# Kernel optimization log

Measured on AMD Instinct MI355X. Metric: run time of the kernel, lower is better.

## Reference

```python
import jax, jax.numpy as jnp
import numpy as np

H = 2048      # hidden_size
NH = 16       # n_heads
DH = H // NH  # d_head = 128
EPS = 1e-5


def layernorm(x, w, b=None, eps=EPS):
    mu = jnp.mean(x, axis=-1, keepdims=True)
    var = jnp.mean(jnp.square(x - mu), axis=-1, keepdims=True)
    y = (x - mu) * jax.lax.rsqrt(var + eps) * w
    return y + b if b is not None else y


def rotate_half(x):
    x1, x2 = jnp.split(x, 2, axis=-1)
    return jnp.concatenate([-x2, x1], axis=-1)


def rotary_cos_sin(seq_len, dim, dtype):
    inv_freq = 1.0 / (10000.0 ** (jnp.arange(0, dim, 2, dtype=jnp.float32) / dim))
    t = jnp.arange(seq_len, dtype=jnp.float32)
    freqs = jnp.outer(t, inv_freq)            # [L, dim/2]
    emb = jnp.concatenate([freqs, freqs], -1) # [L, dim]
    return jnp.cos(emb).astype(dtype), jnp.sin(emb).astype(dtype)


def setup_inputs() -> dict:
    key = jax.random.key(0)
    ks = jax.random.split(key, 9)
    s = 0.02
    return {
        "x": jax.random.normal(ks[0], (4, 2048, H), jnp.float32),
        "ln1_w": jnp.ones((H,), jnp.float32),
        "ln1_b": jnp.zeros((H,), jnp.float32),
        "Wqkv": jax.random.normal(ks[1], (H, 3 * H), jnp.float32) * s,
        "bqkv": jnp.zeros((3 * H,), jnp.float32),
        "qln_w": jnp.ones((H,), jnp.float32),
        "kln_w": jnp.ones((H,), jnp.float32),
        "Wo": jax.random.normal(ks[2], (H, H), jnp.float32) * s,
        "bo": jnp.zeros((H,), jnp.float32),
    }


def reference(x, ln1_w, ln1_b, Wqkv, bqkv, qln_w, kln_w, Wo, bo):
    b, L, _ = x.shape
    # fused LN + QKV projection
    qkv = layernorm(x, ln1_w, ln1_b) @ Wqkv + bqkv          # [b, L, 3H]
    q, k, v = jnp.split(qkv, 3, axis=-1)
    # per-projection LayerNorm (no bias) over full hidden dim
    q = layernorm(q, qln_w).astype(qkv.dtype)
    k = layernorm(k, kln_w).astype(qkv.dtype)
    # rotary on per-head dims: [b, L, NH, DH]
    q = q.reshape(b, L, NH, DH)
    k = k.reshape(b, L, NH, DH)
    cos, sin = rotary_cos_sin(L, DH, q.dtype)
    cos = cos[None, :, None, :]
    sin = sin[None, :, None, :]
    q = q * cos + rotate_half(q) * sin
    k = k * cos + rotate_half(k) * sin
    # b s h d -> b h s d
    q = q.transpose(0, 2, 1, 3)
    k = k.transpose(0, 2, 1, 3)
    v = v.reshape(b, L, NH, DH).transpose(0, 2, 1, 3)
    # SDPA (no mask, non-causal)
    scale = 1.0 / jnp.sqrt(jnp.asarray(DH, q.dtype))
    scores = jnp.einsum('bhqd,bhkd->bhqk', q, k) * scale
    attn = jax.nn.softmax(scores, axis=-1)
    a = jnp.einsum('bhqk,bhkd->bhqd', attn, v)
    a = a.transpose(0, 2, 1, 3).reshape(b, L, H)
    return a @ Wo + bo
```

## Files before the change

kernel.cpp:

```cpp
#include <hip/hip_runtime.h>
#include <math.h>

#define HD   2048
#define NH_  16
#define DH_  128
#define SEQ_ 2048
#define B_   4
#define NT_  (B_*SEQ_)
#define EPS_ 1e-5f

typedef __attribute__((ext_vector_type(8))) __bf16 bf16x8;
typedef __attribute__((ext_vector_type(4))) __bf16 bf16x4;
typedef __attribute__((ext_vector_type(4))) float f32x4;

typedef const __attribute__((address_space(1))) void* gcptr_t;
typedef __attribute__((address_space(3))) void* lptr_t;

__device__ __forceinline__ void gload16(const void* g, void* l) {
  __builtin_amdgcn_global_load_lds((gcptr_t)g, (lptr_t)l, 16, 0, 0);
}

__device__ __forceinline__ float block_sum256(float v, float* red) {
#pragma unroll
  for (int o = 32; o > 0; o >>= 1) v += __shfl_down(v, o);
  int lane = threadIdx.x & 63, wid = threadIdx.x >> 6;
  __syncthreads();
  if (lane == 0) red[wid] = v;
  __syncthreads();
  return red[0] + red[1] + red[2] + red[3];
}

__global__ void ws_diag_kernel(float* out, float v) { out[0] = v; }

__global__ void rope_table_kernel(float* __restrict__ ct, float* __restrict__ st) {
  int i = blockIdx.x * 256 + threadIdx.x;
  if (i >= SEQ_ * 64) return;
  int l = i >> 6, d = i & 63;
  double invf = exp2(-(double)d * (13.287712379549449 / 64.0));
  double ang = (double)l * invf;
  ct[i] = (float)cos(ang);
  st[i] = (float)sin(ang);
}

template<bool LO>
__global__ __launch_bounds__(256) void ln1_split_kernel(const float* __restrict__ x,
    const float* __restrict__ w, const float* __restrict__ bias,
    __bf16* __restrict__ Ah, __bf16* __restrict__ Al) {
  __shared__ float red[4];
  int t = threadIdx.x;
  const float4* xr = (const float4*)(x + (size_t)blockIdx.x * HD);
  float4 a = xr[t], b = xr[t + 256];
  float s = a.x + a.y + a.z + a.w + b.x + b.y + b.z + b.w;
  s = block_sum256(s, red);
  float mu = s * (1.0f / HD);
  float dx[8] = {a.x - mu, a.y - mu, a.z - mu, a.w - mu,
                 b.x - mu, b.y - mu, b.z - mu, b.w - mu};
  float ss = 0.f;
#pragma unroll
  for (int i = 0; i < 8; ++i) ss += dx[i] * dx[i];
  ss = block_sum256(ss, red);
  float rs = rsqrtf(ss * (1.0f / HD) + EPS_);
  float4 w0 = ((const float4*)w)[t], w1 = ((const float4*)w)[t + 256];
  float4 b0 = ((const float4*)bias)[t], b1 = ((const float4*)bias)[t + 256];
  float y[8];
  y[0] = dx[0]*rs*w0.x + b0.x; y[1] = dx[1]*rs*w0.y + b0.y;
  y[2] = dx[2]*rs*w0.z + b0.z; y[3] = dx[3]*rs*w0.w + b0.w;
  y[4] = dx[4]*rs*w1.x + b1.x; y[5] = dx[5]*rs*w1.y + b1.y;
  y[6] = dx[6]*rs*w1.z + b1.z; y[7] = dx[7]*rs*w1.w + b1.w;
  bf16x4 h0, h1, l0, l1;
#pragma unroll
  for (int i = 0; i < 4; ++i) {
    h0[i] = (__bf16)y[i];     l0[i] = (__bf16)(y[i] - (float)h0[i]);
    h1[i] = (__bf16)y[i + 4]; l1[i] = (__bf16)(y[i + 4] - (float)h1[i]);
  }
  size_t base = (size_t)blockIdx.x * HD;
  *(bf16x4*)&Ah[base + 4 * t] = h0;
  *(bf16x4*)&Ah[base + 1024 + 4 * t] = h1;
  if (LO) {
    *(bf16x4*)&Al[base + 4 * t] = l0;
    *(bf16x4*)&Al[base + 1024 + 4 * t] = l1;
  }
}

template<bool LO>
__global__ __launch_bounds__(256) void wsplit_kernel(const float* __restrict__ W,
    int K, int N, __bf16* __restrict__ Wh, __bf16* __restrict__ Wl) {
  __shared__ float ts[64][69];
  int k0 = blockIdx.x << 6, n0 = blockIdx.y << 6;
  int t = threadIdx.x;
#pragma unroll
  for (int i = 0; i < 16; ++i) {
    int lin = t + i * 256;
    int k = lin >> 6, n = lin & 63;
    ts[k][n] = W[(size_t)(k0 + k) * N + n0 + n];
  }
  __syncthreads();
#pragma unroll
  for (int i = 0; i < 16; ++i) {
    int lin = t + i * 256;
    int n = lin >> 6, k = lin & 63;
    float v = ts[k][n];
    __bf16 h = (__bf16)v;
    size_t o = (size_t)(n0 + n) * K + k0 + k;
    Wh[o] = h;
    if (LO) Wl[o] = (__bf16)(v - (float)h);
  }
}

__global__ __launch_bounds__(256) void qkln_rope_kernel(__bf16* __restrict__ qkv,
    const float* __restrict__ qw, const float* __restrict__ kw,
    const float* __restrict__ ct, const float* __restrict__ st) {
  __shared__ float red[4];
  int t = threadIdx.x;
  int tok = blockIdx.x;
  int part = blockIdx.y;
  int pos = tok & (SEQ_ - 1);
  __bf16* base = qkv + (size_t)tok * (3 * HD) + (size_t)part * HD;
  const float* w = part ? kw : qw;
  bf16x8 v8 = *(const bf16x8*)(base + 8 * t);
  float x[8];
#pragma unroll
  for (int i = 0; i < 8; ++i) x[i] = (float)v8[i];
  float s = 0.f;
#pragma unroll
  for (int i = 0; i < 8; ++i) s += x[i];
  s = block_sum256(s, red);
  float mu = s * (1.0f / HD);
  float ss = 0.f;
#pragma unroll
  for (int i = 0; i < 8; ++i) { x[i] -= mu; ss += x[i] * x[i]; }
  ss = block_sum256(ss, red);
  float rs = rsqrtf(ss * (1.0f / HD) + EPS_);
  float4 w0 = *(const float4*)&w[8 * t];
  float4 w1 = *(const float4*)&w[8 * t + 4];
  float y[8];
  y[0] = x[0]*rs*w0.x; y[1] = x[1]*rs*w0.y; y[2] = x[2]*rs*w0.z; y[3] = x[3]*rs*w0.w;
  y[4] = x[4]*rs*w1.x; y[5] = x[5]*rs*w1.y; y[6] = x[6]*rs*w1.z; y[7] = x[7]*rs*w1.w;
  float o[8];
#pragma unroll
  for (int i = 0; i < 8; ++i) o[i] = __shfl_xor(y[i], 8);
  int d = (8 * t) & 127;
  int dd = (d < 64) ? d : d - 64;
  float4 c0 = *(const float4*)&ct[pos * 64 + dd];
  float4 c1 = *(const float4*)&ct[pos * 64 + dd + 4];
  float4 s0 = *(const float4*)&st[pos * 64 + dd];
  float4 s1 = *(const float4*)&st[pos * 64 + dd + 4];
  float cv[8] = {c0.x, c0.y, c0.z, c0.w, c1.x, c1.y, c1.z, c1.w};
  float sv[8] = {s0.x, s0.y, s0.z, s0.w, s1.x, s1.y, s1.z, s1.w};
  bf16x8 o8;
  if (d < 64) {
#pragma unroll
    for (int i = 0; i < 8; ++i) o8[i] = (__bf16)(y[i] * cv[i] - o[i] * sv[i]);
  } else {
#pragma unroll
    for (int i = 0; i < 8; ++i) o8[i] = (__bf16)(y[i] * cv[i] + o[i] * sv[i]);
  }
  *(bf16x8*)(base + 8 * t) = o8;
}

template<int TERMS, bool OUTBF16>
__global__ __launch_bounds__(256, 2) void gemm_bf3_kernel(
    const __bf16* __restrict__ Ah, const __bf16* __restrict__ Al,
    const __bf16* __restrict__ Bh, const __bf16* __restrict__ Bl,
    const float* __restrict__ bias, void* __restrict__ C,
    int M, int N, int K) {
  __shared__ __bf16 lds[TERMS + 1][128][64];
  constexpr int AL_OFF = 16384;
  constexpr int BH_OFF = (TERMS == 1) ? 16384 : 32768;
  constexpr int BL_OFF = 49152;
  const int t = threadIdx.x;
  const int lane = t & 63, wave = t >> 6;
  const int c = lane & 15, g = lane >> 4;
  const int wm = (wave & 1) << 6, wn = (wave >> 1) << 6;

  const int nwg = gridDim.x * gridDim.y;
  int lin = blockIdx.y * gridDim.x + blockIdx.x;
  int swz = (lin & 7) * (nwg >> 3) + (lin >> 3);
  const int col0 = (swz % gridDim.x) << 7;
  const int row0 = (swz / gridDim.x) << 7;

  const int srow = (wave << 5) + (lane >> 3);
  const int ch = lane & 7;
  size_t offA[4], offB[4];
#pragma unroll
  for (int i = 0; i < 4; ++i) {
    int rA = srow + i * 8;
    offA[i] = (size_t)(row0 + rA) * (K * 2) + (size_t)((ch ^ (rA & 7)) << 4);
    offB[i] = (size_t)(col0 + rA) * (K * 2) + (size_t)((ch ^ (rA & 7)) << 4);
  }
  const char* pAh = (const char*)Ah;
  const char* pAl = (const char*)Al;
  const char* pBh = (const char*)Bh;
  const char* pBl = (const char*)Bl;
  char* ldsb = (char*)&lds[0][0][0];

  float bias_[4];
#pragma unroll
  for (int nt = 0; nt < 4; ++nt) bias_[nt] = bias[col0 + wn + nt * 16 + c];

  f32x4 acc[4][4];
#pragma unroll
  for (int mt = 0; mt < 4; ++mt)
#pragma unroll
    for (int nt = 0; nt < 4; ++nt) acc[mt][nt] = f32x4{0.f, 0.f, 0.f, 0.f};

  for (int k0 = 0; k0 < K; k0 += 64) {
    const size_t k2 = (size_t)k0 * 2;
    __syncthreads();
#pragma unroll
    for (int i = 0; i < 4; ++i) {
      const int lr = (wave << 5) + (i << 3);
      gload16(pAh + offA[i] + k2, ldsb + (lr << 7));
      if (TERMS >= 2) gload16(pAl + offA[i] + k2, ldsb + AL_OFF + (lr << 7));
      gload16(pBh + offB[i] + k2, ldsb + BH_OFF + (lr << 7));
      if (TERMS == 3) gload16(pBl + offB[i] + k2, ldsb + BL_OFF + (lr << 7));
    }
    __syncthreads();
#pragma unroll
    for (int kc = 0; kc < 2; ++kc) {
      bf16x8 ah[4], al[4];
#pragma unroll
      for (int mt = 0; mt < 4; ++mt) {
        const int r = wm + mt * 16 + c;
        const int cb = (((kc << 2) | g) ^ (r & 7)) << 4;
        ah[mt] = *(const bf16x8*)(ldsb + (r << 7) + cb);
        if (TERMS >= 2) al[mt] = *(const bf16x8*)(ldsb + AL_OFF + (r << 7) + cb);
      }
#pragma unroll
      for (int nt = 0; nt < 4; ++nt) {
        const int r = wn + nt * 16 + c;
        const int cb = (((kc << 2) | g) ^ (r & 7)) << 4;
        bf16x8 bh = *(const bf16x8*)(ldsb + BH_OFF + (r << 7) + cb);
        bf16x8 bl;
        if (TERMS == 3) bl = *(const bf16x8*)(ldsb + BL_OFF + (r << 7) + cb);
#pragma unroll
        for (int mt = 0; mt < 4; ++mt) {
          acc[mt][nt] = __builtin_amdgcn_mfma_f32_16x16x32_bf16(ah[mt], bh, acc[mt][nt], 0, 0, 0);
          if (TERMS >= 2)
            acc[mt][nt] = __builtin_amdgcn_mfma_f32_16x16x32_bf16(al[mt], bh, acc[mt][nt], 0, 0, 0);
          if (TERMS == 3)
            acc[mt][nt] = __builtin_amdgcn_mfma_f32_16x16x32_bf16(ah[mt], bl, acc[mt][nt], 0, 0, 0);
        }
      }
    }
  }

#pragma unroll
  for (int mt = 0; mt < 4; ++mt) {
#pragma unroll
    for (int r = 0; r < 4; ++r) {
      const size_t row = (size_t)(row0 + wm + mt * 16 + g * 4 + r);
#pragma unroll
      for (int nt = 0; nt < 4; ++nt) {
        float v = acc[mt][nt][r] + bias_[nt];
        size_t idx = row * N + col0 + wn + nt * 16 + c;
        if (OUTBF16) ((__bf16*)C)[idx] = (__bf16)v;
        else         ((float*)C)[idx] = v;
      }
    }
  }
}

__global__ __launch_bounds__(256, 2) void attn_mfma_kernel(
    const __bf16* __restrict__ qkv, __bf16* __restrict__ Oh) {
  __shared__ __bf16 Kb[64 * 128];
  __shared__ __bf16 Vt[128 * 64];
  __shared__ __bf16 Pl[128 * 64];
  const int bh = blockIdx.y, b = bh >> 4, h = bh & 15;
  const int q0 = blockIdx.x << 7;
  const int t = threadIdx.x;
  const int lane = t & 63, wave = t >> 6, g = lane >> 4, c = lane & 15;
  const int wq = wave * 32;
  const size_t rstr = 3 * HD;
  const __bf16* Qg = qkv + (size_t)b * SEQ_ * rstr + (size_t)h * DH_;
  const __bf16* Kg = Qg + HD;
  const __bf16* Vg = Qg + 2 * HD;
  const float SC  = 0.08838834764831845f;
  const float THR = 90.51f;

  bf16x8 qf[2][4];
#pragma unroll
  for (int rt = 0; rt < 2; ++rt) {
    const __bf16* qr = Qg + (size_t)(q0 + wq + rt * 16 + c) * rstr;
#pragma unroll
    for (int kc = 0; kc < 4; ++kc)
      qf[rt][kc] = *(const bf16x8*)(qr + kc * 32 + g * 8);
  }

  f32x4 Oa[2][8];
#pragma unroll
  for (int rt = 0; rt < 2; ++rt)
#pragma unroll
    for (int dt = 0; dt < 8; ++dt) Oa[rt][dt] = f32x4{0.f, 0.f, 0.f, 0.f};
  float m_[2][4], l_[2][4];
#pragma unroll
  for (int rt = 0; rt < 2; ++rt)
#pragma unroll
    for (int r = 0; r < 4; ++r) { m_[rt][r] = -1e30f; l_[rt][r] = 0.f; }

  const int krow = t >> 4;
  const int kch  = t & 15;
  const int kswc = kch ^ (krow & 7);
  const int vkey = t & 63;
  const int vd0  = (t >> 6) * 32;
  const int c7   = c & 7;

  bf16x8 kv[4], vv[4];
#define LOADT(KT)                                                            \
  {                                                                          \
    _Pragma("unroll")                                                        \
    for (int i = 0; i < 4; ++i)                                              \
      kv[i] = *(const bf16x8*)(Kg + (size_t)((KT) + krow + i * 16) * rstr + kch * 8); \
    _Pragma("unroll")                                                        \
    for (int i = 0; i < 4; ++i)                                              \
      vv[i] = *(const bf16x8*)(Vg + (size_t)((KT) + vkey) * rstr + vd0 + i * 8); \
  }
  LOADT(0);

  for (int kt = 0; kt < SEQ_; kt += 64) {
    __syncthreads();
#pragma unroll
    for (int i = 0; i < 4; ++i) {
      *(bf16x8*)&Kb[(krow + i * 16) * 128 + kswc * 8] = kv[i];
#pragma unroll
      for (int j = 0; j < 8; ++j)
        Vt[(vd0 + i * 8 + j) * 64 + (((vkey >> 3) ^ j) << 3) + (vkey & 7)] = vv[i][j];
    }
    __syncthreads();
    if (kt + 64 < SEQ_) LOADT(kt + 64);
    f32x4 Sa[2][4];
#pragma unroll
    for (int rt = 0; rt < 2; ++rt)
#pragma unroll
      for (int nt = 0; nt < 4; ++nt) Sa[rt][nt] = f32x4{0.f, 0.f, 0.f, 0.f};
#pragma unroll
    for (int nt = 0; nt < 4; ++nt) {
      bf16x8 kf[4];
#pragma unroll
      for (int kc = 0; kc < 4; ++kc)
        kf[kc] = *(bf16x8*)&Kb[(nt * 16 + c) * 128 + (((kc * 4 + g) ^ c7) << 3)];
#pragma unroll
      for (int kc = 0; kc < 4; ++kc) {
        Sa[0][nt] = __builtin_amdgcn_mfma_f32_16x16x32_bf16(qf[0][kc], kf[kc], Sa[0][nt], 0, 0, 0);
        Sa[1][nt] = __builtin_amdgcn_mfma_f32_16x16x32_bf16(qf[1][kc], kf[kc], Sa[1][nt], 0, 0, 0);
      }
    }
    float mxv[2][4];
#pragma unroll
    for (int rt = 0; rt < 2; ++rt) {
#pragma unroll
      for (int r = 0; r < 4; ++r) {
        float mx = fmaxf(fmaxf(Sa[rt][0][r], Sa[rt][1][r]),
                         fmaxf(Sa[rt][2][r], Sa[rt][3][r]));
#pragma unroll
        for (int off = 1; off < 16; off <<= 1) mx = fmaxf(mx, __shfl_xor(mx, off));
        mxv[rt][r] = mx;
      }
    }
    bool big = false;
#pragma unroll
    for (int rt = 0; rt < 2; ++rt)
#pragma unroll
      for (int r = 0; r < 4; ++r) big = big || (mxv[rt][r] > m_[rt][r] + THR);
    if (__any(big)) {
      float fs_[2][4];
#pragma unroll
      for (int rt = 0; rt < 2; ++rt) {
#pragma unroll
        for (int r = 0; r < 4; ++r) {
          float mn = fmaxf(m_[rt][r], mxv[rt][r]);
          float fs = __expf((m_[rt][r] - mn) * SC);
          m_[rt][r] = mn;
          l_[rt][r] *= fs;
          fs_[rt][r] = fs;
        }
      }
#pragma unroll
      for (int rt = 0; rt < 2; ++rt)
#pragma unroll
        for (int dt = 0; dt < 8; ++dt)
#pragma unroll
          for (int r = 0; r < 4; ++r) Oa[rt][dt][r] *= fs_[rt][r];
    }
#pragma unroll
    for (int rt = 0; rt < 2; ++rt) {
#pragma unroll
      for (int r = 0; r < 4; ++r) {
        const float mn = m_[rt][r];
        const int prow = wq + rt * 16 + 4 * g + r;
        const int psw = prow & 7;
        float ps = 0.f;
#pragma unroll
        for (int nt = 0; nt < 4; ++nt) {
          float p = __expf((Sa[rt][nt][r] - mn) * SC);
          Pl[prow * 64 + (((nt * 2 + (c >> 3)) ^ psw) << 3) + (c & 7)] = (__bf16)p;
          ps += p;
        }
#pragma unroll
        for (int off = 1; off < 16; off <<= 1) ps += __shfl_xor(ps, off);
        l_[rt][r] += ps;
      }
    }
#pragma unroll
    for (int k2 = 0; k2 < 2; ++k2) {
      const int pch = ((k2 * 4 + g) ^ c7) << 3;
      bf16x8 pf0 = *(bf16x8*)&Pl[(wq + c) * 64 + pch];
      bf16x8 pf1 = *(bf16x8*)&Pl[(wq + 16 + c) * 64 + pch];
#pragma unroll
      for (int dt = 0; dt < 8; ++dt) {
        bf16x8 vf = *(bf16x8*)&Vt[(dt * 16 + c) * 64 + pch];
        Oa[0][dt] = __builtin_amdgcn_mfma_f32_16x16x32_bf16(pf0, vf, Oa[0][dt], 0, 0, 0);
        Oa[1][dt] = __builtin_amdgcn_mfma_f32_16x16x32_bf16(pf1, vf, Oa[1][dt], 0, 0, 0);
      }
    }
  }
#undef LOADT
#pragma unroll
  for (int rt = 0; rt < 2; ++rt) {
#pragma unroll
    for (int r = 0; r < 4; ++r) {
      float inv = 1.0f / l_[rt][r];
      size_t obase = (size_t)(b * SEQ_ + q0 + wq + rt * 16 + 4 * g + r) * HD + h * DH_;
#pragma unroll
      for (int dt = 0; dt < 8; ++dt)
        Oh[obase + dt * 16 + c] = (__bf16)(Oa[rt][dt][r] * inv);
    }
  }
}

extern "C" void kernel_launch(void* const* d_in, const int* in_sizes, int n_in,
                              void* d_out, int out_size, void* d_ws, size_t ws_size,
                              hipStream_t stream) {
  const float* x    = (const float*)d_in[0];
  const float* ln1w = (const float*)d_in[1];
  const float* ln1b = (const float*)d_in[2];
  const float* Wqkv = (const float*)d_in[3];
  const float* bqkv = (const float*)d_in[4];
  const float* qlnw = (const float*)d_in[5];
  const float* klnw = (const float*)d_in[6];
  const float* Wo   = (const float*)d_in[7];
  const float* bo   = (const float*)d_in[8];
  float* out = (float*)d_out;

  const size_t qkv_b = (size_t)NT_ * 3 * HD * 2;
  const size_t a_b   = (size_t)NT_ * HD * 2;
  const size_t w_b   = (size_t)3 * HD * HD * 2;
  const size_t t_b   = (size_t)SEQ_ * 64 * 4;
  const size_t need  = qkv_b + 2 * a_b + 2 * w_b + 2 * t_b;
  if (ws_size < need) {
    ws_diag_kernel<<<1, 1, 0, stream>>>(out, (float)(ws_size >> 20));
    return;
  }
  char* w = (char*)d_ws;
  __bf16* qkvb = (__bf16*)w;              w += qkv_b;
  __bf16* Ah   = (__bf16*)w;              w += a_b;
  __bf16* Al   = (__bf16*)w;              w += a_b;
  __bf16* Wth  = (__bf16*)w;              w += w_b;
  __bf16* Wtl  = (__bf16*)w;              w += w_b;
  float*  ctab = (float*)w;               w += t_b;
  float*  stab = (float*)w;

  rope_table_kernel<<<(SEQ_ * 64 + 255) / 256, 256, 0, stream>>>(ctab, stab);
  ln1_split_kernel<false><<<NT_, 256, 0, stream>>>(x, ln1w, ln1b, Ah, Al);
  wsplit_kernel<false><<<dim3(HD / 64, 3 * HD / 64), 256, 0, stream>>>(
      Wqkv, HD, 3 * HD, Wth, Wtl);
  gemm_bf3_kernel<1, true><<<dim3(3 * HD / 128, NT_ / 128), 256, 0, stream>>>(
      Ah, nullptr, Wth, nullptr, bqkv, qkvb, NT_, 3 * HD, HD);
  qkln_rope_kernel<<<dim3(NT_, 2), 256, 0, stream>>>(
      qkvb, qlnw, klnw, ctab, stab);
  wsplit_kernel<false><<<dim3(HD / 64, HD / 64), 256, 0, stream>>>(
      Wo, HD, HD, Wth, Wtl);
  attn_mfma_kernel<<<dim3(SEQ_ / 128, B_ * NH_), 256, 0, stream>>>(
      qkvb, Ah);
  gemm_bf3_kernel<1, false><<<dim3(HD / 128, NT_ / 128), 256, 0, stream>>>(
      Ah, nullptr, Wth, nullptr, bo, out, NT_, HD, HD);
}
```

Before: 702.8 us.

## Alias K and P LDS buffers, drop register prefetch, vectorize V transpose

The attention kernel now reuses one shared buffer for the K tile and the softmax probabilities, with an extra barrier between the QK^T reads and the P writes. This cuts LDS per block from 48KB to 32KB. The register-held prefetch of the next K/V tile is removed, and V is loaded as 4-element chunks and transposed so each thread does 16-byte LDS writes instead of scalar scatters. The exponentials switch from __expf to exp2f with the log2e factor folded into the scale. The aim is lower LDS and register pressure and cheaper V staging, at the cost of no longer overlapping global loads with compute and adding a third barrier per tile.

```diff
diff --git a/kernel.cpp b/kernel.cpp
--- a/kernel.cpp
+++ b/kernel.cpp
@@ -263,9 +263,8 @@
 
 __global__ __launch_bounds__(256, 2) void attn_mfma_kernel(
     const __bf16* __restrict__ qkv, __bf16* __restrict__ Oh) {
-  __shared__ __bf16 Kb[64 * 128];
+  __shared__ __bf16 KbPl[64 * 128];
   __shared__ __bf16 Vt[128 * 64];
-  __shared__ __bf16 Pl[128 * 64];
   const int bh = blockIdx.y, b = bh >> 4, h = bh & 15;
   const int q0 = blockIdx.x << 7;
   const int t = threadIdx.x;
@@ -275,8 +274,8 @@
   const __bf16* Qg = qkv + (size_t)b * SEQ_ * rstr + (size_t)h * DH_;
   const __bf16* Kg = Qg + HD;
   const __bf16* Vg = Qg + 2 * HD;
-  const float SC  = 0.08838834764831845f;
-  const float THR = 90.51f;
+  const float SCL2 = 0.12754374742764546f;
+  const float THR  = 90.51f;
 
   bf16x8 qf[2][4];
 #pragma unroll
@@ -298,36 +297,35 @@
 #pragma unroll
     for (int r = 0; r < 4; ++r) { m_[rt][r] = -1e30f; l_[rt][r] = 0.f; }
 
-  const int krow = t >> 4;
-  const int kch  = t & 15;
-  const int kswc = kch ^ (krow & 7);
-  const int vkey = t & 63;
-  const int vd0  = (t >> 6) * 32;
-  const int c7   = c & 7;
-
-  bf16x8 kv[4], vv[4];
-#define LOADT(KT)                                                            \
-  {                                                                          \
-    _Pragma("unroll")                                                        \
-    for (int i = 0; i < 4; ++i)                                              \
-      kv[i] = *(const bf16x8*)(Kg + (size_t)((KT) + krow + i * 16) * rstr + kch * 8); \
-    _Pragma("unroll")                                                        \
-    for (int i = 0; i < 4; ++i)                                              \
-      vv[i] = *(const bf16x8*)(Vg + (size_t)((KT) + vkey) * rstr + vd0 + i * 8); \
-  }
-  LOADT(0);
+  const int krow  = t >> 4;
+  const int kch   = t & 15;
+  const int kswc  = kch ^ (krow & 7);
+  const int vkb   = t & 7;
+  const int vdimq = t >> 3;
+  const int c7    = c & 7;
 
   for (int kt = 0; kt < SEQ_; kt += 64) {
+    bf16x8 kv[4];
+#pragma unroll
+    for (int i = 0; i < 4; ++i)
+      kv[i] = *(const bf16x8*)(Kg + (size_t)(kt + krow + i * 16) * rstr + kch * 8);
+    bf16x4 vv4[8];
+#pragma unroll
+    for (int j = 0; j < 8; ++j)
+      vv4[j] = *(const bf16x4*)(Vg + (size_t)(kt + vkb * 8 + j) * rstr + vdimq * 4);
     __syncthreads();
 #pragma unroll
-    for (int i = 0; i < 4; ++i) {
-      *(bf16x8*)&Kb[(krow + i * 16) * 128 + kswc * 8] = kv[i];
-#pragma unroll
-      for (int j = 0; j < 8; ++j)
-        Vt[(vd0 + i * 8 + j) * 64 + (((vkey >> 3) ^ j) << 3) + (vkey & 7)] = vv[i][j];
+    for (int i = 0; i < 4; ++i)
+      *(bf16x8*)&KbPl[(krow + i * 16) * 128 + kswc * 8] = kv[i];
+#pragma unroll
+    for (int dd = 0; dd < 4; ++dd) {
+      bf16x8 wr;
+#pragma unroll
+      for (int j = 0; j < 8; ++j) wr[j] = vv4[j][dd];
+      const int row = vdimq * 4 + dd;
+      *(bf16x8*)&Vt[row * 64 + ((vkb ^ (row & 7)) << 3)] = wr;
     }
     __syncthreads();
-    if (kt + 64 < SEQ_) LOADT(kt + 64);
     f32x4 Sa[2][4];
 #pragma unroll
     for (int rt = 0; rt < 2; ++rt)
@@ -338,7 +336,7 @@
       bf16x8 kf[4];
 #pragma unroll
       for (int kc = 0; kc < 4; ++kc)
-        kf[kc] = *(bf16x8*)&Kb[(nt * 16 + c) * 128 + (((kc * 4 + g) ^ c7) << 3)];
+        kf[kc] = *(bf16x8*)&KbPl[(nt * 16 + c) * 128 + (((kc * 4 + g) ^ c7) << 3)];
 #pragma unroll
       for (int kc = 0; kc < 4; ++kc) {
         Sa[0][nt] = __builtin_amdgcn_mfma_f32_16x16x32_bf16(qf[0][kc], kf[kc], Sa[0][nt], 0, 0, 0);
@@ -357,6 +355,7 @@
         mxv[rt][r] = mx;
       }
     }
+    __syncthreads();
     bool big = false;
 #pragma unroll
     for (int rt = 0; rt < 2; ++rt)
@@ -369,7 +368,7 @@
 #pragma unroll
         for (int r = 0; r < 4; ++r) {
           float mn = fmaxf(m_[rt][r], mxv[rt][r]);
-          float fs = __expf((m_[rt][r] - mn) * SC);
+          float fs = exp2f((m_[rt][r] - mn) * SCL2);
           m_[rt][r] = mn;
           l_[rt][r] *= fs;
           fs_[rt][r] = fs;
@@ -392,8 +391,8 @@
         float ps = 0.f;
 #pragma unroll
         for (int nt = 0; nt < 4; ++nt) {
-          float p = __expf((Sa[rt][nt][r] - mn) * SC);
-          Pl[prow * 64 + (((nt * 2 + (c >> 3)) ^ psw) << 3) + (c & 7)] = (__bf16)p;
+          float p = exp2f((Sa[rt][nt][r] - mn) * SCL2);
+          KbPl[prow * 64 + (((nt * 2 + (c >> 3)) ^ psw) << 3) + (c & 7)] = (__bf16)p;
           ps += p;
         }
 #pragma unroll
@@ -404,8 +403,8 @@
 #pragma unroll
     for (int k2 = 0; k2 < 2; ++k2) {
       const int pch = ((k2 * 4 + g) ^ c7) << 3;
-      bf16x8 pf0 = *(bf16x8*)&Pl[(wq + c) * 64 + pch];
-      bf16x8 pf1 = *(bf16x8*)&Pl[(wq + 16 + c) * 64 + pch];
+      bf16x8 pf0 = *(bf16x8*)&KbPl[(wq + c) * 64 + pch];
+      bf16x8 pf1 = *(bf16x8*)&KbPl[(wq + 16 + c) * 64 + pch];
 #pragma unroll
       for (int dt = 0; dt < 8; ++dt) {
         bf16x8 vf = *(bf16x8*)&Vt[(dt * 16 + c) * 64 + pch];
@@ -414,7 +413,6 @@
       }
     }
   }
-#undef LOADT
 #pragma unroll
   for (int rt = 0; rt < 2; ++rt) {
 #pragma unroll
```

Result: slower. 738.4 us (+5.1%).

## Compute softmax row sums via MFMA with ones and defer max rescale on overflow

Applied to the files above, without the earlier changes.

The per-tile row-max shuffle reduction is removed. Probabilities are computed against the stale running max, and a rescale runs only when some exponent exceeds a cap. Row sums are accumulated by an MFMA of the bf16 P tile against a ones vector instead of shuffle reductions, which also makes the normalizer match the bf16-rounded P used for the output. The cost is two extra MFMAs per k-chunk and a recompute path when the cap is hit, in exchange for removing many cross-lane shuffles per tile.

```diff
diff --git a/kernel.cpp b/kernel.cpp
--- a/kernel.cpp
+++ b/kernel.cpp
@@ -275,8 +275,11 @@
   const __bf16* Qg = qkv + (size_t)b * SEQ_ * rstr + (size_t)h * DH_;
   const __bf16* Kg = Qg + HD;
   const __bf16* Vg = Qg + 2 * HD;
-  const float SC  = 0.08838834764831845f;
-  const float THR = 90.51f;
+  const float SC   = 0.08838834764831845f;
+  const float PCAP = 2980.0f;
+
+  const __bf16 one_ = (__bf16)1.0f;
+  const bf16x8 ones8 = {one_, one_, one_, one_, one_, one_, one_, one_};
 
   bf16x8 qf[2][4];
 #pragma unroll
@@ -292,11 +295,12 @@
   for (int rt = 0; rt < 2; ++rt)
 #pragma unroll
     for (int dt = 0; dt < 8; ++dt) Oa[rt][dt] = f32x4{0.f, 0.f, 0.f, 0.f};
-  float m_[2][4], l_[2][4];
+  f32x4 ls[2] = {f32x4{0.f, 0.f, 0.f, 0.f}, f32x4{0.f, 0.f, 0.f, 0.f}};
+  float m_[2][4];
 #pragma unroll
   for (int rt = 0; rt < 2; ++rt)
 #pragma unroll
-    for (int r = 0; r < 4; ++r) { m_[rt][r] = -1e30f; l_[rt][r] = 0.f; }
+    for (int r = 0; r < 4; ++r) m_[rt][r] = -1e30f;
 
   const int krow = t >> 4;
   const int kch  = t & 15;
@@ -345,43 +349,7 @@
         Sa[1][nt] = __builtin_amdgcn_mfma_f32_16x16x32_bf16(qf[1][kc], kf[kc], Sa[1][nt], 0, 0, 0);
       }
     }
-    float mxv[2][4];
-#pragma unroll
-    for (int rt = 0; rt < 2; ++rt) {
-#pragma unroll
-      for (int r = 0; r < 4; ++r) {
-        float mx = fmaxf(fmaxf(Sa[rt][0][r], Sa[rt][1][r]),
-                         fmaxf(Sa[rt][2][r], Sa[rt][3][r]));
-#pragma unroll
-        for (int off = 1; off < 16; off <<= 1) mx = fmaxf(mx, __shfl_xor(mx, off));
-        mxv[rt][r] = mx;
-      }
-    }
-    bool big = false;
-#pragma unroll
-    for (int rt = 0; rt < 2; ++rt)
-#pragma unroll
-      for (int r = 0; r < 4; ++r) big = big || (mxv[rt][r] > m_[rt][r] + THR);
-    if (__any(big)) {
-      float fs_[2][4];
-#pragma unroll
-      for (int rt = 0; rt < 2; ++rt) {
-#pragma unroll
-        for (int r = 0; r < 4; ++r) {
-          float mn = fmaxf(m_[rt][r], mxv[rt][r]);
-          float fs = __expf((m_[rt][r] - mn) * SC);
-          m_[rt][r] = mn;
-          l_[rt][r] *= fs;
-          fs_[rt][r] = fs;
-        }
-      }
-#pragma unroll
-      for (int rt = 0; rt < 2; ++rt)
-#pragma unroll
-        for (int dt = 0; dt < 8; ++dt)
-#pragma unroll
-          for (int r = 0; r < 4; ++r) Oa[rt][dt][r] *= fs_[rt][r];
-    }
+    float pmax = 0.f;
 #pragma unroll
     for (int rt = 0; rt < 2; ++rt) {
 #pragma unroll
@@ -389,16 +357,51 @@
         const float mn = m_[rt][r];
         const int prow = wq + rt * 16 + 4 * g + r;
         const int psw = prow & 7;
-        float ps = 0.f;
 #pragma unroll
         for (int nt = 0; nt < 4; ++nt) {
           float p = __expf((Sa[rt][nt][r] - mn) * SC);
+          pmax = fmaxf(pmax, p);
           Pl[prow * 64 + (((nt * 2 + (c >> 3)) ^ psw) << 3) + (c & 7)] = (__bf16)p;
-          ps += p;
         }
-#pragma unroll
-        for (int off = 1; off < 16; off <<= 1) ps += __shfl_xor(ps, off);
-        l_[rt][r] += ps;
+      }
+    }
+    if (__any(pmax > PCAP)) {
+      float fs_[2][4];
+#pragma unroll
+      for (int rt = 0; rt < 2; ++rt) {
+#pragma unroll
+        for (int r = 0; r < 4; ++r) {
+          float mx = fmaxf(fmaxf(Sa[rt][0][r], Sa[rt][1][r]),
+                           fmaxf(Sa[rt][2][r], Sa[rt][3][r]));
+#pragma unroll
+          for (int off = 1; off < 16; off <<= 1) mx = fmaxf(mx, __shfl_xor(mx, off));
+          float mn = fmaxf(m_[rt][r], mx);
+          fs_[rt][r] = __expf((m_[rt][r] - mn) * SC);
+          m_[rt][r] = mn;
+        }
+      }
+#pragma unroll
+      for (int rt = 0; rt < 2; ++rt) {
+        ls[rt][0] *= fs_[rt][0]; ls[rt][1] *= fs_[rt][1];
+        ls[rt][2] *= fs_[rt][2]; ls[rt][3] *= fs_[rt][3];
+#pragma unroll
+        for (int dt = 0; dt < 8; ++dt)
+#pragma unroll
+          for (int r = 0; r < 4; ++r) Oa[rt][dt][r] *= fs_[rt][r];
+      }
+#pragma unroll
+      for (int rt = 0; rt < 2; ++rt) {
+#pragma unroll
+        for (int r = 0; r < 4; ++r) {
+          const float mn = m_[rt][r];
+          const int prow = wq + rt * 16 + 4 * g + r;
+          const int psw = prow & 7;
+#pragma unroll
+          for (int nt = 0; nt < 4; ++nt) {
+            float p = __expf((Sa[rt][nt][r] - mn) * SC);
+            Pl[prow * 64 + (((nt * 2 + (c >> 3)) ^ psw) << 3) + (c & 7)] = (__bf16)p;
+          }
+        }
       }
     }
 #pragma unroll
@@ -406,6 +409,8 @@
       const int pch = ((k2 * 4 + g) ^ c7) << 3;
       bf16x8 pf0 = *(bf16x8*)&Pl[(wq + c) * 64 + pch];
       bf16x8 pf1 = *(bf16x8*)&Pl[(wq + 16 + c) * 64 + pch];
+      ls[0] = __builtin_amdgcn_mfma_f32_16x16x32_bf16(pf0, ones8, ls[0], 0, 0, 0);
+      ls[1] = __builtin_amdgcn_mfma_f32_16x16x32_bf16(pf1, ones8, ls[1], 0, 0, 0);
 #pragma unroll
       for (int dt = 0; dt < 8; ++dt) {
         bf16x8 vf = *(bf16x8*)&Vt[(dt * 16 + c) * 64 + pch];
@@ -419,7 +424,7 @@
   for (int rt = 0; rt < 2; ++rt) {
 #pragma unroll
     for (int r = 0; r < 4; ++r) {
-      float inv = 1.0f / l_[rt][r];
+      float inv = 1.0f / ls[rt][r];
       size_t obase = (size_t)(b * SEQ_ + q0 + wq + rt * 16 + 4 * g + r) * HD + h * DH_;
 #pragma unroll
       for (int dt = 0; dt < 8; ++dt)
```

After: 602.3 us. -14.3%, faster.
